# Optimization experiments

Measured on AMD Instinct MI355X. Metric: run time of the kernel, lower is better.

## Reference

```python
import jax, jax.numpy as jnp
import numpy as np

B = 20000      # edges
LMAX = 4
MMAX = 2
CIN = 64
COUT = 64
ECH = 128      # edge_channels
L1 = LMAX + 1
M1 = MMAX + 1
TOUT = COUT + LMAX * COUT          # out + gate channels = 320
ROUT = L1 * M1 * 2 * CIN           # radial MLP output size = 1920


def setup_inputs() -> dict:
    key = jax.random.key(0)
    ks = jax.random.split(key, 10)
    s = 0.05
    return {
        "x": jax.random.normal(ks[0], (B, L1, M1, 2, CIN), jnp.float32),
        "x_edge": jax.random.normal(ks[1], (B, ECH), jnp.float32),
        "W_r": jax.random.normal(ks[2], (M1, CIN, TOUT), jnp.float32) * s,
        "W_i": jax.random.normal(ks[3], (M1, CIN, TOUT), jnp.float32) * s,
        "w1": jax.random.normal(ks[4], (ECH, ECH), jnp.float32) * s,
        "b1": jnp.zeros((ECH,), jnp.float32),
        "ln_g": jnp.ones((ECH,), jnp.float32),
        "ln_b": jnp.zeros((ECH,), jnp.float32),
        "w2": jax.random.normal(ks[5], (ECH, ROUT), jnp.float32) * s,
        "b2": jnp.zeros((ROUT,), jnp.float32),
    }


def reference(x, x_edge, W_r, W_i, w1, b1, ln_g, ln_b, w2, b2):
    # Radial MLP: Linear -> LayerNorm -> SiLU -> Linear
    h = x_edge @ w1 + b1
    mu = jnp.mean(h, axis=-1, keepdims=True)
    var = jnp.mean((h - mu) ** 2, axis=-1, keepdims=True)
    h = (h - mu) / jnp.sqrt(var + 1e-5) * ln_g + ln_b
    h = jax.nn.silu(h)
    rad = (h @ w2 + b2).reshape(B, L1, M1, 2, CIN)
    # Edge-modulated input scaling
    xs = x * rad
    # Complex weight tensor [M1, R, r, CIN, TOUT]: [[W_r, -W_i], [W_i, W_r]]
    W = jnp.stack([jnp.stack([W_r, -W_i], axis=1),
                   jnp.stack([W_i, W_r], axis=1)], axis=1)
    out = jnp.einsum('blmrc,mRrco->blmRo', xs, W)
    # Mask invalid (l, m) positions where m > l
    lm_mask = (jnp.arange(L1)[:, None] >= jnp.arange(M1)[None, :]).astype(out.dtype)
    out = out * lm_mask[None, :, :, None, None]
    # Zero imaginary component at m = 0
    m0_mask = jnp.ones((1, 1, M1, 2, 1), out.dtype).at[:, :, 0, 1, :].set(0.0)
    out = out * m0_mask
    # Gate channels only non-zero at (l=0, m=0, real)
    gate_mask = (jnp.ones((1, L1, M1, 2, TOUT), out.dtype)
                 .at[..., COUT:].set(0.0)
                 .at[:, 0, 0, 0, COUT:].set(1.0))
    out = out * gate_mask
    return out
```

## Files before the change

### kernel.cpp

```cpp
#include <hip/hip_runtime.h>

#define NEDGE 20000
#define ECH   128
#define RAD   1920
#define OPE   9600
#define BE    16

typedef short bf16x8 __attribute__((ext_vector_type(8)));
typedef float f32x4  __attribute__((ext_vector_type(4)));

__device__ __forceinline__ unsigned short f2bf(float f) {
  unsigned u = __float_as_uint(f);
  u += 0x7fffu + ((u >> 16) & 1u);
  return (unsigned short)(u >> 16);
}

__device__ __forceinline__ void ldsbar() {
  asm volatile("s_waitcnt lgkmcnt(0)" ::: "memory");
  __builtin_amdgcn_s_barrier();
}

__global__ __launch_bounds__(256) void prep_kernel(
    const float* __restrict__ w1, const float* __restrict__ w2,
    const float* __restrict__ Wr, const float* __restrict__ Wi,
    unsigned short* __restrict__ ws) {
  int gid = blockIdx.x * 256 + threadIdx.x;
  unsigned short* w1t = ws;
  unsigned short* w2t = ws + 16384;
  unsigned short* wt  = ws + 16384 + 245760;
  if (gid < 16384) {
    int k = gid >> 7, n = gid & 127;
    w1t[n * 128 + k] = f2bf(w1[gid]);
  } else if (gid < 16384 + 245760) {
    int i = gid - 16384;
    int k = i / 1920, n = i - k * 1920;
    w2t[n * 128 + k] = f2bf(w2[i]);
  } else if (gid < 16384 + 245760 + 61440) {
    int i = gid - (16384 + 245760);
    int o = i % 320, mc = i / 320;
    int c = mc & 63, m = mc >> 6;
    float vr = Wr[i], vi = Wi[i];
    size_t b0 = ((size_t)((m * 2 + 0) * 320 + o)) * 128;
    size_t b1 = ((size_t)((m * 2 + 1) * 320 + o)) * 128;
    wt[b0 + c]      = f2bf(vr);
    wt[b0 + 64 + c] = f2bf(-vi);
    wt[b1 + c]      = f2bf(vi);
    wt[b1 + 64 + c] = f2bf(vr);
  }
}

template<int N4>
__device__ __forceinline__ void zwrite(float* __restrict__ outb, int tid, int s4) {
  const f32x4 z4 = {0.f, 0.f, 0.f, 0.f};
  for (int p = tid; p < N4 * BE; p += 256) {
    int e = p / N4, f = p - e * N4;
    __builtin_nontemporal_store(z4, (f32x4*)(outb + (size_t)e * OPE) + (s4 + f));
  }
}

__global__ __launch_bounds__(256, 4) void fused_kernel(
    const float* __restrict__ x,  const float* __restrict__ xe,
    const float* __restrict__ b1, const float* __restrict__ lng,
    const float* __restrict__ lnb, const float* __restrict__ b2,
    const unsigned short* __restrict__ ws, float* __restrict__ out) {

  const unsigned short* w1t = ws;
  const unsigned short* w2t = ws + 16384;
  const unsigned short* wt  = ws + 16384 + 245760;

  __shared__ unsigned short xsb[BE][136];
  __shared__ unsigned short hb[BE][136];
  __shared__ float hp[BE][132];

  const int tid  = threadIdx.x;
  const int wave = tid >> 6, lane = tid & 63;
  const int lq = lane >> 4, lr = lane & 15;
  const int eb = blockIdx.x / 3, slab = blockIdx.x % 3;
  const int e0 = eb * BE;
  const int n0 = wave * 32;

  static const signed char lmtab[3][4] = {{0, 3, 6, 9}, {12, 4, 7, 8}, {10, 11, 13, 14}};
  const signed char* lms = lmtab[slab];

  auto PF = [&](int lm, float* a, float* b, float& c0, float& c1) {
#pragma unroll
    for (int i = 0; i < 4; ++i) {
      const float* xrow = x + (size_t)(e0 + 4 * lq + i) * RAD + lm * 128;
      a[i] = xrow[n0 + lr];
      b[i] = xrow[n0 + 16 + lr];
    }
    c0 = b2[lm * 128 + n0 + lr];
    c1 = b2[lm * 128 + n0 + 16 + lr];
  };

  float pfa[4][4], pfb[4][4], pc0[4], pc1[4];

  PF(lms[0], pfa[0], pfb[0], pc0[0], pc1[0]);

  for (int s = tid; s < BE * 32; s += 256) {
    int e = s >> 5, k4 = s & 31;
    float4 v = *((const float4*)(xe + (size_t)(e0 + e) * ECH) + k4);
    ushort4 u;
    u.x = f2bf(v.x); u.y = f2bf(v.y); u.z = f2bf(v.z); u.w = f2bf(v.w);
    *(ushort4*)&xsb[e][k4 * 4] = u;
  }

  {
    float* ob = out + (size_t)e0 * OPE;
    if (slab == 0) {
      zwrite<240>(ob, tid, 80);
      zwrite<144>(ob, tid, 496);
      zwrite<144>(ob, tid, 976);
      zwrite<144>(ob, tid, 1456);
    } else if (slab == 1) {
      zwrite<160>(ob, tid, 320);
      zwrite<64>(ob, tid, 656);  zwrite<64>(ob, tid, 736);
      zwrite<64>(ob, tid, 1136); zwrite<64>(ob, tid, 1216);
      zwrite<64>(ob, tid, 1296); zwrite<64>(ob, tid, 1376);
      zwrite<144>(ob, tid, 1936);
    } else {
      zwrite<160>(ob, tid, 800);
      zwrite<64>(ob, tid, 1616); zwrite<64>(ob, tid, 1696);
      zwrite<64>(ob, tid, 1776); zwrite<64>(ob, tid, 1856);
      zwrite<64>(ob, tid, 2096); zwrite<64>(ob, tid, 2176);
      zwrite<64>(ob, tid, 2256); zwrite<64>(ob, tid, 2336);
    }
  }
  ldsbar();

  {
    f32x4 c0 = {0.f, 0.f, 0.f, 0.f}, c1 = {0.f, 0.f, 0.f, 0.f};
#pragma unroll
    for (int ks = 0; ks < 4; ++ks) {
      bf16x8 a  = *(const bf16x8*)&xsb[lr][lq * 8 + ks * 32];
      bf16x8 bA = *(const bf16x8*)(w1t + (size_t)(n0 + lr) * 128 + lq * 8 + ks * 32);
      bf16x8 bB = *(const bf16x8*)(w1t + (size_t)(n0 + 16 + lr) * 128 + lq * 8 + ks * 32);
      c0 = __builtin_amdgcn_mfma_f32_16x16x32_bf16(a, bA, c0, 0, 0, 0);
      c1 = __builtin_amdgcn_mfma_f32_16x16x32_bf16(a, bB, c1, 0, 0, 0);
    }
    float bb0 = b1[n0 + lr], bb1 = b1[n0 + 16 + lr];
#pragma unroll
    for (int i = 0; i < 4; ++i) {
      int e = 4 * lq + i;
      hp[e][n0 + lr]      = c0[i] + bb0;
      hp[e][n0 + 16 + lr] = c1[i] + bb1;
    }
  }
  ldsbar();

  {
    int e = tid >> 4, j = tid & 15;
    float v[8];
    float4 a = *((const float4*)&hp[e][j * 8]);
    float4 b = *((const float4*)&hp[e][j * 8 + 4]);
    v[0] = a.x; v[1] = a.y; v[2] = a.z; v[3] = a.w;
    v[4] = b.x; v[5] = b.y; v[6] = b.z; v[7] = b.w;
    float s = 0.f, q = 0.f;
#pragma unroll
    for (int i = 0; i < 8; ++i) { s += v[i]; q += v[i] * v[i]; }
#pragma unroll
    for (int mk = 1; mk <= 8; mk <<= 1) {
      s += __shfl_xor(s, mk, 64);
      q += __shfl_xor(q, mk, 64);
    }
    float mean = s * (1.f / 128.f);
    float var  = q * (1.f / 128.f) - mean * mean;
    float rstd = rsqrtf(var + 1e-5f);
    float4 g0 = *((const float4*)&lng[j * 8]), g1 = *((const float4*)&lng[j * 8 + 4]);
    float4 t0 = *((const float4*)&lnb[j * 8]), t1 = *((const float4*)&lnb[j * 8 + 4]);
    float gg[8] = {g0.x, g0.y, g0.z, g0.w, g1.x, g1.y, g1.z, g1.w};
    float bb[8] = {t0.x, t0.y, t0.z, t0.w, t1.x, t1.y, t1.z, t1.w};
    ushort4 o0, o1;
    unsigned short uo[8];
#pragma unroll
    for (int i = 0; i < 8; ++i) {
      float hn = (v[i] - mean) * rstd * gg[i] + bb[i];
      float sv = hn / (1.f + __expf(-hn));
      uo[i] = f2bf(sv);
    }
    o0.x = uo[0]; o0.y = uo[1]; o0.z = uo[2]; o0.w = uo[3];
    o1.x = uo[4]; o1.y = uo[5]; o1.z = uo[6]; o1.w = uo[7];
    *(ushort4*)&hb[e][j * 8]     = o0;
    *(ushort4*)&hb[e][j * 8 + 4] = o1;
  }
  ldsbar();

  bf16x8 hfr[4];
#pragma unroll
  for (int ks = 0; ks < 4; ++ks) hfr[ks] = *(const bf16x8*)&hb[lr][lq * 8 + ks * 32];

#pragma unroll
  for (int vi = 0; vi < 4; ++vi) {
    const int lm = lms[vi];
    const int m = lm % 3;

    if (vi < 3) PF(lms[vi + 1], pfa[vi + 1], pfb[vi + 1], pc0[vi + 1], pc1[vi + 1]);

    f32x4 r0 = {0.f, 0.f, 0.f, 0.f}, r1 = {0.f, 0.f, 0.f, 0.f};
    const unsigned short* w2base = w2t + (size_t)(lm * 128) * 128;
#pragma unroll
    for (int ks = 0; ks < 4; ++ks) {
      bf16x8 b0 = *(const bf16x8*)(w2base + (size_t)(n0 + lr) * 128 + lq * 8 + ks * 32);
      bf16x8 b1v = *(const bf16x8*)(w2base + (size_t)(n0 + 16 + lr) * 128 + lq * 8 + ks * 32);
      r0 = __builtin_amdgcn_mfma_f32_16x16x32_bf16(hfr[ks], b0, r0, 0, 0, 0);
      r1 = __builtin_amdgcn_mfma_f32_16x16x32_bf16(hfr[ks], b1v, r1, 0, 0, 0);
    }
#pragma unroll
    for (int i = 0; i < 4; ++i) {
      int e = 4 * lq + i;
      xsb[e][n0 + lr]      = f2bf((r0[i] + pc0[vi]) * pfa[vi][i]);
      xsb[e][n0 + 16 + lr] = f2bf((r1[i] + pc1[vi]) * pfb[vi][i]);
    }
    ldsbar();

    bf16x8 afr[4];
#pragma unroll
    for (int ks = 0; ks < 4; ++ks) afr[ks] = *(const bf16x8*)&xsb[lr][lq * 8 + ks * 32];

    const int totT = (lm == 0) ? 20 : ((m == 0) ? 4 : 8);
    for (int t = wave; t < totT; t += 4) {
      int R, o0v;
      if (lm == 0) { R = 0; o0v = t * 16; }
      else         { R = t >> 2; o0v = (t & 3) * 16; }
      const unsigned short* wb = wt + ((size_t)((m * 2 + R) * 320) + o0v) * 128;
      f32x4 acc = {0.f, 0.f, 0.f, 0.f};
#pragma unroll
      for (int ks = 0; ks < 4; ++ks) {
        bf16x8 b = *(const bf16x8*)(wb + (size_t)lr * 128 + lq * 8 + ks * 32);
        acc = __builtin_amdgcn_mfma_f32_16x16x32_bf16(afr[ks], b, acc, 0, 0, 0);
      }
      float* ob = out + (size_t)(e0 + 4 * lq) * OPE + lm * 640 + R * 320 + o0v + lr;
      __builtin_nontemporal_store(acc[0], ob + 0 * OPE);
      __builtin_nontemporal_store(acc[1], ob + 1 * OPE);
      __builtin_nontemporal_store(acc[2], ob + 2 * OPE);
      __builtin_nontemporal_store(acc[3], ob + 3 * OPE);
    }
    ldsbar();
  }
}

extern "C" void kernel_launch(void* const* d_in, const int* in_sizes, int n_in,
                              void* d_out, int out_size, void* d_ws, size_t ws_size,
                              hipStream_t stream) {
  const float* x   = (const float*)d_in[0];
  const float* xe  = (const float*)d_in[1];
  const float* Wr  = (const float*)d_in[2];
  const float* Wi  = (const float*)d_in[3];
  const float* w1  = (const float*)d_in[4];
  const float* b1  = (const float*)d_in[5];
  const float* lng = (const float*)d_in[6];
  const float* lnb = (const float*)d_in[7];
  const float* w2  = (const float*)d_in[8];
  const float* b2  = (const float*)d_in[9];
  float* out = (float*)d_out;
  unsigned short* ws = (unsigned short*)d_ws;

  const int prepN = 16384 + 245760 + 61440;
  prep_kernel<<<(prepN + 255) / 256, 256, 0, stream>>>(w1, w2, Wr, Wi, ws);
  fused_kernel<<<(NEDGE / BE) * 3, 256, 0, stream>>>(x, xe, b1, lng, lnb, b2, ws, out);
}
```

Measured before the change: 183.8 us.

## Interleave zero-fill stores with compute and vectorize output stores via transposed MFMA

The zero-fill of masked output regions moves out of the kernel prologue and is spread across the four lm iterations, so its stores overlap with the MFMA work. The final MFMA swaps its operands so each lane holds four consecutive output channels, which turns four scalar strided stores into one 16-byte vector store. Nontemporal stores become regular stores, and the slab-1 lm order is changed. The intent is to cut store-path stalls and write traffic, at the risk of extra cache pollution from the regular stores.

```diff
diff --git a/kernel.cpp b/kernel.cpp
--- a/kernel.cpp
+++ b/kernel.cpp
@@ -54,7 +54,7 @@
   const f32x4 z4 = {0.f, 0.f, 0.f, 0.f};
   for (int p = tid; p < N4 * BE; p += 256) {
     int e = p / N4, f = p - e * N4;
-    __builtin_nontemporal_store(z4, (f32x4*)(outb + (size_t)e * OPE) + (s4 + f));
+    *((f32x4*)(outb + (size_t)e * OPE) + (s4 + f)) = z4;
   }
 }
 
@@ -79,7 +79,7 @@
   const int e0 = eb * BE;
   const int n0 = wave * 32;
 
-  static const signed char lmtab[3][4] = {{0, 3, 6, 9}, {12, 4, 7, 8}, {10, 11, 13, 14}};
+  static const signed char lmtab[3][4] = {{0, 3, 6, 9}, {4, 7, 8, 12}, {10, 11, 13, 14}};
   const signed char* lms = lmtab[slab];
 
   auto PF = [&](int lm, float* a, float* b, float& c0, float& c1) {
@@ -94,7 +94,6 @@
   };
 
   float pfa[4][4], pfb[4][4], pc0[4], pc1[4];
-
   PF(lms[0], pfa[0], pfb[0], pc0[0], pc1[0]);
 
   for (int s = tid; s < BE * 32; s += 256) {
@@ -103,28 +102,6 @@
     ushort4 u;
     u.x = f2bf(v.x); u.y = f2bf(v.y); u.z = f2bf(v.z); u.w = f2bf(v.w);
     *(ushort4*)&xsb[e][k4 * 4] = u;
-  }
-
-  {
-    float* ob = out + (size_t)e0 * OPE;
-    if (slab == 0) {
-      zwrite<240>(ob, tid, 80);
-      zwrite<144>(ob, tid, 496);
-      zwrite<144>(ob, tid, 976);
-      zwrite<144>(ob, tid, 1456);
-    } else if (slab == 1) {
-      zwrite<160>(ob, tid, 320);
-      zwrite<64>(ob, tid, 656);  zwrite<64>(ob, tid, 736);
-      zwrite<64>(ob, tid, 1136); zwrite<64>(ob, tid, 1216);
-      zwrite<64>(ob, tid, 1296); zwrite<64>(ob, tid, 1376);
-      zwrite<144>(ob, tid, 1936);
-    } else {
-      zwrite<160>(ob, tid, 800);
-      zwrite<64>(ob, tid, 1616); zwrite<64>(ob, tid, 1696);
-      zwrite<64>(ob, tid, 1776); zwrite<64>(ob, tid, 1856);
-      zwrite<64>(ob, tid, 2096); zwrite<64>(ob, tid, 2176);
-      zwrite<64>(ob, tid, 2256); zwrite<64>(ob, tid, 2336);
-    }
   }
   ldsbar();
 
@@ -189,6 +166,8 @@
 #pragma unroll
   for (int ks = 0; ks < 4; ++ks) hfr[ks] = *(const bf16x8*)&hb[lr][lq * 8 + ks * 32];
 
+  float* const obase = out + (size_t)e0 * OPE;
+
 #pragma unroll
   for (int vi = 0; vi < 4; ++vi) {
     const int lm = lms[vi];
@@ -226,14 +205,29 @@
       f32x4 acc = {0.f, 0.f, 0.f, 0.f};
 #pragma unroll
       for (int ks = 0; ks < 4; ++ks) {
-        bf16x8 b = *(const bf16x8*)(wb + (size_t)lr * 128 + lq * 8 + ks * 32);
-        acc = __builtin_amdgcn_mfma_f32_16x16x32_bf16(afr[ks], b, acc, 0, 0, 0);
+        bf16x8 aw = *(const bf16x8*)(wb + (size_t)lr * 128 + lq * 8 + ks * 32);
+        acc = __builtin_amdgcn_mfma_f32_16x16x32_bf16(aw, afr[ks], acc, 0, 0, 0);
       }
-      float* ob = out + (size_t)(e0 + 4 * lq) * OPE + lm * 640 + R * 320 + o0v + lr;
-      __builtin_nontemporal_store(acc[0], ob + 0 * OPE);
-      __builtin_nontemporal_store(acc[1], ob + 1 * OPE);
-      __builtin_nontemporal_store(acc[2], ob + 2 * OPE);
-      __builtin_nontemporal_store(acc[3], ob + 3 * OPE);
+      *(f32x4*)(obase + (size_t)lr * OPE + lm * 640 + R * 320 + o0v + lq * 4) = acc;
+    }
+
+    if (slab == 0) {
+      if (vi == 0) zwrite<240>(obase, tid, 80);
+      if (vi == 1) zwrite<144>(obase, tid, 496);
+      if (vi == 2) zwrite<144>(obase, tid, 976);
+      if (vi == 3) zwrite<144>(obase, tid, 1456);
+    } else if (slab == 1) {
+      if (vi == 0) { zwrite<64>(obase, tid, 656);  zwrite<64>(obase, tid, 736);
+                     zwrite<160>(obase, tid, 320); }
+      if (vi == 1) { zwrite<64>(obase, tid, 1136); zwrite<64>(obase, tid, 1216); }
+      if (vi == 2) { zwrite<64>(obase, tid, 1296); zwrite<64>(obase, tid, 1376); }
+      if (vi == 3) zwrite<144>(obase, tid, 1936);
+    } else {
+      if (vi == 0) { zwrite<64>(obase, tid, 1616); zwrite<64>(obase, tid, 1696);
+                     zwrite<160>(obase, tid, 800); }
+      if (vi == 1) { zwrite<64>(obase, tid, 1776); zwrite<64>(obase, tid, 1856); }
+      if (vi == 2) { zwrite<64>(obase, tid, 2096); zwrite<64>(obase, tid, 2176); }
+      if (vi == 3) { zwrite<64>(obase, tid, 2256); zwrite<64>(obase, tid, 2336); }
     }
     ldsbar();
   }
```

Result: slower. 297.1 us (+61.6%).
